# Optimization experiments

Hardware: AMD Instinct MI355X
Metric: run time of the kernel (lower is better)

## Reference

```python
import jax, jax.numpy as jnp
import numpy as np

B, S, E = 32, 577, 1024
H = 16
D = E // H  # head_size = 64


def setup_inputs() -> dict:
    key = jax.random.key(0)
    ks = jax.random.split(key, 5)
    scale_init = E ** -0.5
    x = jax.random.normal(ks[0], (B, S, E), dtype=jnp.float32)
    # Per-head projection weights. torch Linear weight is [out,in]; we store
    # [H, E, D] so that x @ Wq[h] == torch_linear(x) with weight Wq[h].T.
    Wq = jax.random.normal(ks[1], (H, E, D), dtype=jnp.float32) * scale_init
    Wk = jax.random.normal(ks[2], (H, E, D), dtype=jnp.float32) * scale_init
    Wv = jax.random.normal(ks[3], (H, E, D), dtype=jnp.float32) * scale_init
    # Output projection (with bias, as in nn.Linear default)
    Wo = jax.random.normal(ks[4], (E, E), dtype=jnp.float32) * scale_init
    bo = jnp.zeros((E,), dtype=jnp.float32)
    return {"x": x, "Wq": Wq, "Wk": Wk, "Wv": Wv, "Wo": Wo, "bo": bo}


def reference(x, Wq, Wk, Wv, Wo, bo):
    scale = D ** -0.5
    # Per-head QKV projections, vectorized over heads: [B,H,S,D]
    q = jnp.einsum('bse,hed->bhsd', x, Wq)
    k = jnp.einsum('bse,hed->bhsd', x, Wk)
    v = jnp.einsum('bse,hed->bhsd', x, Wv)
    scores = jnp.einsum('bhsd,bhtd->bhst', q, k) * scale  # [B,H,S,S]
    attn = jax.nn.softmax(scores, axis=-1)
    out = jnp.einsum('bhst,bhtd->bhsd', attn, v)  # [B,H,S,D]
    # Concat heads: head h occupies slice [h*D:(h+1)*D], matching torch.cat order
    out = out.transpose(0, 2, 1, 3).reshape(B, S, E)
    return out @ Wo.T + bo  # torch Linear: x @ W.T + b
```

## Files before the change

kernel.cpp:

```cpp
#include <hip/hip_runtime.h>
#include <hip/hip_bf16.h>
#include <stdint.h>

using sh8    = __attribute__((ext_vector_type(8))) short;
using f32x4  = __attribute__((ext_vector_type(4))) float;
using f32x16 = __attribute__((ext_vector_type(16))) float;

#define MFMA16(a, b, c) __builtin_amdgcn_mfma_f32_16x16x32_bf16(a, b, c, 0, 0, 0)
#define EXP2F(x) __builtin_amdgcn_exp2f(x)

static constexpr int BB = 32, SS = 577, HH = 16;
static constexpr int MM = BB * SS;
static constexpr int SPAD = 640;
static constexpr float QSCALE = 0.18033688011112042f;

__device__ __forceinline__ ushort f2b(float f) {
  union { float f; uint32_t u; } v{f};
  uint32_t r = v.u + 0x7FFFu + ((v.u >> 16) & 1u);
  return (ushort)(r >> 16);
}

#if __has_builtin(__builtin_amdgcn_cvt_pk_bf16_f32)
typedef __attribute__((ext_vector_type(2))) __bf16 bf16x2_t;
__device__ __forceinline__ uint32_t pk_bf16(float a, float b) {
  union { bf16x2_t v; uint32_t u; } c;
  c.v = __builtin_amdgcn_cvt_pk_bf16_f32(a, b);
  return c.u;
}
#else
__device__ __forceinline__ uint32_t pk_bf16(float a, float b) {
  return (uint32_t)f2b(a) | ((uint32_t)f2b(b) << 16);
}
#endif

__device__ __forceinline__ void gld16(const ushort* g, ushort* l) {
  __builtin_amdgcn_global_load_lds(
      (const __attribute__((address_space(1))) uint32_t*)g,
      (__attribute__((address_space(3))) uint32_t*)l, 16, 0, 0);
}

__global__ __launch_bounds__(256)
void convert2_f32_bf16(const float* __restrict__ a, ushort* __restrict__ oa, int na4,
                       const float* __restrict__ b, ushort* __restrict__ ob, int nb4) {
  const int total = na4 + nb4;
  const int stride = gridDim.x * 256;
  for (int i = blockIdx.x * 256 + threadIdx.x; i < total; i += stride) {
    const float4 f = (i < na4) ? ((const float4*)a)[i] : ((const float4*)b)[i - na4];
    ushort4 u;
    u.x = f2b(f.x); u.y = f2b(f.y); u.z = f2b(f.z); u.w = f2b(f.w);
    if (i < na4) ((ushort4*)oa)[i] = u;
    else         ((ushort4*)ob)[i - na4] = u;
  }
}

__global__ __launch_bounds__(256)
void convert_wqkv(const float* __restrict__ Wq, const float* __restrict__ Wk,
                  const float* __restrict__ Wv, ushort* __restrict__ Wt) {
  __shared__ ushort T[64 * 72];
  const int tid = threadIdx.x;
  const int kt = blockIdx.x, sh = blockIdx.y;
  const int sel = sh >> 4, h = sh & 15;
  const float* W = (sel == 0) ? Wq : ((sel == 1) ? Wk : Wv);
  const float qs = (sel == 0) ? QSCALE : 1.0f;
  const int rr = tid >> 4;
  const int rc = (tid & 15) * 4;
#pragma unroll
  for (int p = 0; p < 64; p += 16) {
    const float4 f = *(const float4*)(W + (size_t)h * 65536 + (size_t)(kt * 64 + p + rr) * 64 + rc);
    ushort4 u;
    u.x = f2b(f.x * qs); u.y = f2b(f.y * qs); u.z = f2b(f.z * qs); u.w = f2b(f.w * qs);
    *(ushort4*)&T[(p + rr) * 72 + rc] = u;
  }
  __syncthreads();
  const int dd = tid >> 2;
  const int c16 = (tid & 3) * 16;
  sh8 v0, v1;
#pragma unroll
  for (int j = 0; j < 8; j++) v0[j] = (short)T[(c16 + j) * 72 + dd];
#pragma unroll
  for (int j = 0; j < 8; j++) v1[j] = (short)T[(c16 + 8 + j) * 72 + dd];
  ushort* op = Wt + ((size_t)sel * 1024 + h * 64 + dd) * 1024 + kt * 64 + c16;
  *(sh8*)op = v0;
  *(sh8*)(op + 8) = v1;
}

template <int MODE>
__global__ __launch_bounds__(256)
void gemm_bt(const ushort* __restrict__ A, const ushort* __restrict__ Bt,
             ushort* __restrict__ Cb, float* __restrict__ Cf,
             const float* __restrict__ bias, int M, int N, int K) {
  __shared__ ushort Al[128 * 64];
  __shared__ ushort Bl[128 * 64];
  const int tid = threadIdx.x;
  const int lane = tid & 63, w = tid >> 6;
  const int l15 = lane & 15, quad = lane >> 4;
  const int wm = (w >> 1) * 64, wn = (w & 1) * 64;
  const int m0 = blockIdx.y * 128, n0 = blockIdx.x * 128;

  f32x4 acc[4][4];
#pragma unroll
  for (int i = 0; i < 4; i++)
#pragma unroll
    for (int j = 0; j < 4; j++) acc[i][j] = f32x4{0.f, 0.f, 0.f, 0.f};

  const int rbase = tid >> 3;
  const int swzc = ((tid & 7) ^ (rbase & 7)) * 8;
  const ushort* Ag[4]; const ushort* Bg[4];
  ushort* lA[4]; ushort* lB[4];
#pragma unroll
  for (int i = 0; i < 4; i++) {
    Ag[i] = A + (size_t)min(m0 + i * 32 + rbase, M - 1) * K + swzc;
    Bg[i] = Bt + (size_t)(n0 + i * 32 + rbase) * K + swzc;
    lA[i] = &Al[(i * 256 + tid) * 8];
    lB[i] = &Bl[(i * 256 + tid) * 8];
  }
  const int swz = l15 & 7;
  const int c0 = (quad ^ swz) * 8;
  const int c1 = ((quad + 4) ^ swz) * 8;
  const int arow = (wm + l15) * 64;
  const int brow = (wn + l15) * 64;

  for (int k0 = 0; k0 < K; k0 += 64) {
    __syncthreads();
#pragma unroll
    for (int i = 0; i < 4; i++) {
      gld16(Ag[i] + k0, lA[i]);
      gld16(Bg[i] + k0, lB[i]);
    }
    __syncthreads();
#pragma unroll
    for (int kc = 0; kc < 2; kc++) {
      const int ck = (kc == 0) ? c0 : c1;
      sh8 af[4], bfr[4];
#pragma unroll
      for (int i = 0; i < 4; i++) af[i] = *(const sh8*)&Al[arow + i * 1024 + ck];
#pragma unroll
      for (int j = 0; j < 4; j++) bfr[j] = *(const sh8*)&Bl[brow + j * 1024 + ck];
#pragma unroll
      for (int i = 0; i < 4; i++)
#pragma unroll
        for (int j = 0; j < 4; j++) acc[i][j] = MFMA16(bfr[j], af[i], acc[i][j]);
    }
  }

#pragma unroll
  for (int i = 0; i < 4; i++) {
    const int row = m0 + wm + i * 16 + l15;
    const bool ok = row < M;
#pragma unroll
    for (int j = 0; j < 4; j++) {
      const int col0 = n0 + wn + j * 16 + quad * 4;
      if (MODE == 0) {
        uint2 pk;
        pk.x = pk_bf16(acc[i][j][0], acc[i][j][1]);
        pk.y = pk_bf16(acc[i][j][2], acc[i][j][3]);
        if (ok) *(uint2*)&Cb[(size_t)row * N + col0] = pk;
      } else {
        const float4 b4 = *(const float4*)&bias[col0];
        float4 v;
        v.x = acc[i][j][0] + b4.x; v.y = acc[i][j][1] + b4.y;
        v.z = acc[i][j][2] + b4.z; v.w = acc[i][j][3] + b4.w;
        if (ok) *(float4*)&Cf[(size_t)row * N + col0] = v;
      }
    }
  }
}

__global__ __launch_bounds__(256)
void transpose_v(const ushort* __restrict__ QKV, ushort* __restrict__ Vtg) {
  __shared__ ushort T[64 * 72];
  const int tid = threadIdx.x;
  const int st = blockIdx.x, bh = blockIdx.y;
  const int b = bh >> 4, h = bh & 15;
  const int sr = tid >> 3;
  const int sc = (tid & 7) * 8;
#pragma unroll
  for (int p = 0; p < 64; p += 32) {
    const int s = st * 64 + p + sr;
    uint4 d = uint4{0u, 0u, 0u, 0u};
    if (s < SS) d = *(const uint4*)(QKV + ((size_t)b * SS + s) * 3072 + 2048 + h * 64 + sc);
    *(uint4*)&T[(p + sr) * 72 + sc] = d;
  }
  __syncthreads();
  const int dd = tid >> 2;
  const int s16 = (tid & 3) * 16;
  sh8 v0, v1;
#pragma unroll
  for (int j = 0; j < 8; j++) v0[j] = (short)T[(s16 + j) * 72 + dd];
#pragma unroll
  for (int j = 0; j < 8; j++) v1[j] = (short)T[(s16 + 8 + j) * 72 + dd];
  ushort* outp = Vtg + ((size_t)bh * 64 + dd) * SPAD + st * 64 + s16;
  *(sh8*)outp = v0;
  *(sh8*)(outp + 8) = v1;
}

__global__ __launch_bounds__(256)
void flash_attn(const ushort* __restrict__ QKV, const ushort* __restrict__ Vtg,
                ushort* __restrict__ Ob) {
  __shared__ ushort Kl[64 * 64];
  __shared__ ushort Vl[64 * 64];
  __shared__ ushort Pl[128 * 72];
  const int tid = threadIdx.x;
  const int lane = tid & 63, w = tid >> 6;
  const int l15 = lane & 15, quad = lane >> 4;
  const int qb = blockIdx.x, bh = blockIdx.y;
  const int b = bh >> 4, h = bh & 15;

  sh8 qf[2][2];
#pragma unroll
  for (int g = 0; g < 2; g++) {
    const int qr = qb * 128 + w * 32 + g * 16 + l15;
    const ushort* qrow = QKV + ((size_t)b * SS + min(qr, SS - 1)) * 3072 + h * 64;
    qf[g][0] = *(const sh8*)(qrow + quad * 8);
    qf[g][1] = *(const sh8*)(qrow + 32 + quad * 8);
  }

  sh8 ones;
#pragma unroll
  for (int j = 0; j < 8; j++) ones[j] = (short)0x3F80;

  f32x4 o[2][4];
  f32x4 acc_l[2];
#pragma unroll
  for (int g = 0; g < 2; g++) {
    acc_l[g] = f32x4{0.f, 0.f, 0.f, 0.f};
#pragma unroll
    for (int t = 0; t < 4; t++) o[g][t] = f32x4{0.f, 0.f, 0.f, 0.f};
  }

  const int r0 = tid >> 3;
  const int swzs = ((tid & 7) ^ (r0 & 7)) * 8;
  const ushort* Kg = QKV + (size_t)b * SS * 3072 + 1024 + h * 64 + swzs;
  const ushort* Vg0 = Vtg + ((size_t)bh * 64 + r0) * SPAD + swzs;
  const ushort* Vg1 = Vtg + ((size_t)bh * 64 + 32 + r0) * SPAD + swzs;
  ushort* lK0 = &Kl[tid * 8];
  ushort* lK1 = &Kl[(256 + tid) * 8];
  ushort* lV0 = &Vl[tid * 8];
  ushort* lV1 = &Vl[(256 + tid) * 8];

  const int swz = l15 & 7;
  const int ca0 = (quad ^ swz) * 8;
  const int ca1 = ((quad + 4) ^ swz) * 8;
  ushort* plw[2] = { &Pl[(w * 32 + l15) * 72], &Pl[(w * 32 + 16 + l15) * 72] };

  for (int kt = 0; kt < 10; kt++) {
    const int kb = kt * 64;
    __syncthreads();
    gld16(Kg + (size_t)min(kb + r0, SS - 1) * 3072, lK0);
    gld16(Kg + (size_t)min(kb + 32 + r0, SS - 1) * 3072, lK1);
    gld16(Vg0 + kb, lV0);
    gld16(Vg1 + kb, lV1);
    __syncthreads();

#pragma unroll
    for (int tn = 0; tn < 4; tn++) {
      const int kr = tn * 16 + l15;
      const sh8 k0 = *(const sh8*)&Kl[kr * 64 + ca0];
      const sh8 k1 = *(const sh8*)&Kl[kr * 64 + ca1];
#pragma unroll
      for (int g = 0; g < 2; g++) {
        f32x4 s = f32x4{0.f, 0.f, 0.f, 0.f};
        s = MFMA16(k0, qf[g][0], s);
        s = MFMA16(k1, qf[g][1], s);
        if (kt == 9) {
#pragma unroll
          for (int r = 0; r < 4; r++)
            if ((tn * 16 + quad * 4 + r) != 0) s[r] = -1e30f;
        }
        uint2 pp;
        pp.x = pk_bf16(EXP2F(s[0]), EXP2F(s[1]));
        pp.y = pk_bf16(EXP2F(s[2]), EXP2F(s[3]));
        *(uint2*)(plw[g] + tn * 16 + quad * 4) = pp;
      }
    }
    sh8 pa[2][2];
#pragma unroll
    for (int g = 0; g < 2; g++) {
      pa[g][0] = *(const sh8*)(plw[g] + quad * 8);
      pa[g][1] = *(const sh8*)(plw[g] + 32 + quad * 8);
      acc_l[g] = MFMA16(ones, pa[g][0], acc_l[g]);
      acc_l[g] = MFMA16(ones, pa[g][1], acc_l[g]);
    }
#pragma unroll
    for (int t = 0; t < 4; t++) {
      const int vr = t * 16 + l15;
      const sh8 v0 = *(const sh8*)&Vl[vr * 64 + ca0];
      const sh8 v1 = *(const sh8*)&Vl[vr * 64 + ca1];
#pragma unroll
      for (int g = 0; g < 2; g++) {
        o[g][t] = MFMA16(v0, pa[g][0], o[g][t]);
        o[g][t] = MFMA16(v1, pa[g][1], o[g][t]);
      }
    }
  }

#pragma unroll
  for (int g = 0; g < 2; g++) {
    const float inv = 1.0f / acc_l[g][0];
    const int s = qb * 128 + w * 32 + g * 16 + l15;
    if (s < SS) {
      ushort* op = Ob + ((size_t)b * SS + s) * 1024 + h * 64 + quad * 4;
#pragma unroll
      for (int t = 0; t < 4; t++) {
        uint2 ov;
        ov.x = pk_bf16(o[g][t][0] * inv, o[g][t][1] * inv);
        ov.y = pk_bf16(o[g][t][2] * inv, o[g][t][3] * inv);
        *(uint2*)(op + t * 16) = ov;
      }
    }
  }
}

extern "C" void kernel_launch(void* const* d_in, const int* in_sizes, int n_in,
                              void* d_out, int out_size, void* d_ws, size_t ws_size,
                              hipStream_t stream) {
  const float* x  = (const float*)d_in[0];
  const float* Wq = (const float*)d_in[1];
  const float* Wk = (const float*)d_in[2];
  const float* Wv = (const float*)d_in[3];
  const float* Wo = (const float*)d_in[4];
  const float* bo = (const float*)d_in[5];
  float* out = (float*)d_out;

  ushort* Xb  = (ushort*)d_ws;
  ushort* Wt  = Xb  + (size_t)MM * 1024;
  ushort* Wob = Wt  + (size_t)3072 * 1024;
  ushort* QKV = Wob + (size_t)1024 * 1024;
  ushort* Vtg = QKV + (size_t)MM * 3072;
  ushort* Ob  = Xb;

  convert2_f32_bf16<<<4096, 256, 0, stream>>>(x, Xb, MM * 1024 / 4, Wo, Wob, 1024 * 1024 / 4);
  convert_wqkv<<<dim3(16, 48), 256, 0, stream>>>(Wq, Wk, Wv, Wt);
  gemm_bt<0><<<dim3(24, 145), 256, 0, stream>>>(Xb, Wt, QKV, nullptr, nullptr, MM, 3072, 1024);
  transpose_v<<<dim3(10, 512), 256, 0, stream>>>(QKV, Vtg);
  flash_attn<<<dim3(5, 512), 256, 0, stream>>>(QKV, Vtg, Ob);
  gemm_bt<1><<<dim3(8, 145), 256, 0, stream>>>(Ob, Wob, nullptr, out, bo, MM, 1024, 1024);
}
```

Before: 457.3 us.

## Double-buffer K/V tiles in flash attention and remap GEMM workgroups

The flash attention kernel now keeps two LDS buffers for K and V and prefetches the next key tile while computing on the current one, which removes one barrier per iteration and overlaps global loads with MFMA work. Separately, the GEMM kernel remaps linear workgroup IDs with a stride-8 permutation, apparently so that concurrently scheduled blocks share A/B tiles in cache across XCDs. The cost is doubled K/V shared memory, which may lower occupancy. The remap assumes the number of workgroups is divisible by 8.

```diff
diff --git a/kernel.cpp b/kernel.cpp
--- a/kernel.cpp
+++ b/kernel.cpp
@@ -95,7 +95,12 @@
   const int lane = tid & 63, w = tid >> 6;
   const int l15 = lane & 15, quad = lane >> 4;
   const int wm = (w >> 1) * 64, wn = (w & 1) * 64;
-  const int m0 = blockIdx.y * 128, n0 = blockIdx.x * 128;
+
+  const int nwg = gridDim.x * gridDim.y;
+  const int orig = blockIdx.y * gridDim.x + blockIdx.x;
+  const int wgid = (orig & 7) * (nwg >> 3) + (orig >> 3);
+  const int m0 = (wgid / gridDim.x) * 128;
+  const int n0 = (wgid % gridDim.x) * 128;
 
   f32x4 acc[4][4];
 #pragma unroll
@@ -197,8 +202,8 @@
 __global__ __launch_bounds__(256)
 void flash_attn(const ushort* __restrict__ QKV, const ushort* __restrict__ Vtg,
                 ushort* __restrict__ Ob) {
-  __shared__ ushort Kl[64 * 64];
-  __shared__ ushort Vl[64 * 64];
+  __shared__ ushort Kl[2][64 * 64];
+  __shared__ ushort Vl[2][64 * 64];
   __shared__ ushort Pl[128 * 72];
   const int tid = threadIdx.x;
   const int lane = tid & 63, w = tid >> 6;
@@ -233,30 +238,39 @@
   const ushort* Kg = QKV + (size_t)b * SS * 3072 + 1024 + h * 64 + swzs;
   const ushort* Vg0 = Vtg + ((size_t)bh * 64 + r0) * SPAD + swzs;
   const ushort* Vg1 = Vtg + ((size_t)bh * 64 + 32 + r0) * SPAD + swzs;
-  ushort* lK0 = &Kl[tid * 8];
-  ushort* lK1 = &Kl[(256 + tid) * 8];
-  ushort* lV0 = &Vl[tid * 8];
-  ushort* lV1 = &Vl[(256 + tid) * 8];
+  ushort* lK0[2] = { &Kl[0][tid * 8],         &Kl[1][tid * 8] };
+  ushort* lK1[2] = { &Kl[0][(256 + tid) * 8], &Kl[1][(256 + tid) * 8] };
+  ushort* lV0[2] = { &Vl[0][tid * 8],         &Vl[1][tid * 8] };
+  ushort* lV1[2] = { &Vl[0][(256 + tid) * 8], &Vl[1][(256 + tid) * 8] };
 
   const int swz = l15 & 7;
   const int ca0 = (quad ^ swz) * 8;
   const int ca1 = ((quad + 4) ^ swz) * 8;
   ushort* plw[2] = { &Pl[(w * 32 + l15) * 72], &Pl[(w * 32 + 16 + l15) * 72] };
 
+  gld16(Kg + (size_t)min(r0, SS - 1) * 3072, lK0[0]);
+  gld16(Kg + (size_t)min(32 + r0, SS - 1) * 3072, lK1[0]);
+  gld16(Vg0, lV0[0]);
+  gld16(Vg1, lV1[0]);
+  __syncthreads();
+
   for (int kt = 0; kt < 10; kt++) {
-    const int kb = kt * 64;
-    __syncthreads();
-    gld16(Kg + (size_t)min(kb + r0, SS - 1) * 3072, lK0);
-    gld16(Kg + (size_t)min(kb + 32 + r0, SS - 1) * 3072, lK1);
-    gld16(Vg0 + kb, lV0);
-    gld16(Vg1 + kb, lV1);
-    __syncthreads();
+    const int cur = kt & 1;
+    if (kt < 9) {
+      const int kb1 = (kt + 1) * 64;
+      gld16(Kg + (size_t)min(kb1 + r0, SS - 1) * 3072, lK0[cur ^ 1]);
+      gld16(Kg + (size_t)min(kb1 + 32 + r0, SS - 1) * 3072, lK1[cur ^ 1]);
+      gld16(Vg0 + kb1, lV0[cur ^ 1]);
+      gld16(Vg1 + kb1, lV1[cur ^ 1]);
+    }
+    const ushort* Kc = &Kl[cur][0];
+    const ushort* Vc = &Vl[cur][0];
 
 #pragma unroll
     for (int tn = 0; tn < 4; tn++) {
       const int kr = tn * 16 + l15;
-      const sh8 k0 = *(const sh8*)&Kl[kr * 64 + ca0];
-      const sh8 k1 = *(const sh8*)&Kl[kr * 64 + ca1];
+      const sh8 k0 = *(const sh8*)&Kc[kr * 64 + ca0];
+      const sh8 k1 = *(const sh8*)&Kc[kr * 64 + ca1];
 #pragma unroll
       for (int g = 0; g < 2; g++) {
         f32x4 s = f32x4{0.f, 0.f, 0.f, 0.f};
@@ -284,14 +298,16 @@
 #pragma unroll
     for (int t = 0; t < 4; t++) {
       const int vr = t * 16 + l15;
-      const sh8 v0 = *(const sh8*)&Vl[vr * 64 + ca0];
-      const sh8 v1 = *(const sh8*)&Vl[vr * 64 + ca1];
+      const sh8 v0 = *(const sh8*)&Vc[vr * 64 + ca0];
+      const sh8 v1 = *(const sh8*)&Vc[vr * 64 + ca1];
 #pragma unroll
       for (int g = 0; g < 2; g++) {
         o[g][t] = MFMA16(v0, pa[g][0], o[g][t]);
         o[g][t] = MFMA16(v1, pa[g][1], o[g][t]);
       }
     }
+
+    if (kt < 9) __syncthreads();
   }
 
 #pragma unroll
```

New measurement: 439.8 us. 1.04x faster.
